# Kernel optimization log

Measured on AMD Instinct MI355X. Metric: run time of the kernel, lower is better.

## Reference

```python
import jax, jax.numpy as jnp
import numpy as np

B, N, D, H = 8, 2048, 128, 8
HD = D // H  # head_depth = 16
CLIP = 10.0
INF = 1e10
THETA = 10000.0
SCALE_BASE = 512.0
LOGIT_SCALE = float(np.log(400.0) / np.log(50.0) / np.sqrt(HD))


def _rotate_half(x):
    # interleaved pairs: (x1, x2) -> (-x2, x1)
    x1 = x[..., ::2]
    x2 = x[..., 1::2]
    return jnp.stack((-x2, x1), axis=-1).reshape(x.shape)


def _rope_xpos(n, hd):
    # rotary_embedding_torch RotaryEmbedding(dim=hd, use_xpos=True)
    inv_freq = 1.0 / (THETA ** (jnp.arange(0, hd, 2, dtype=jnp.float32) / hd))  # (hd/2,)
    t = jnp.arange(n, dtype=jnp.float32)
    freqs = t[:, None] * inv_freq[None, :]          # (n, hd/2)
    freqs = jnp.repeat(freqs, 2, axis=-1)           # (n, hd) interleaved dup
    sc = (jnp.arange(0, hd, 2, dtype=jnp.float32) + 0.4 * hd) / (1.4 * hd)  # (hd/2,)
    power = (t - (n // 2)) / SCALE_BASE             # centered positions
    scale = sc[None, :] ** power[:, None]           # (n, hd/2)
    scale = jnp.repeat(scale, 2, axis=-1)           # (n, hd)
    return freqs, scale


def setup_inputs() -> dict:
    key = jax.random.key(0)
    ks = jax.random.split(key, 7)
    stdv_qkv = 1.0 / np.sqrt(HD)
    stdv_out = 1.0 / np.sqrt(D)
    q = jax.random.normal(ks[0], (B, N, D), dtype=jnp.float32)
    k = jax.random.normal(ks[1], (B, N, D), dtype=jnp.float32)
    v = jax.random.normal(ks[2], (B, N, D), dtype=jnp.float32)
    Wq = jax.random.uniform(ks[3], (D, D), minval=-stdv_qkv, maxval=stdv_qkv, dtype=jnp.float32)
    Wk = jax.random.uniform(ks[4], (D, D), minval=-stdv_qkv, maxval=stdv_qkv, dtype=jnp.float32)
    Wv = jax.random.uniform(ks[5], (D, D), minval=-stdv_qkv, maxval=stdv_qkv, dtype=jnp.float32)
    Wout = jax.random.uniform(ks[6], (D, D), minval=-stdv_out, maxval=stdv_out, dtype=jnp.float32)
    mask = jnp.zeros((B, N, 1), dtype=bool)
    return {"q": q, "k": k, "v": v, "Wq": Wq, "Wk": Wk, "Wv": Wv, "Wout": Wout, "mask": mask}


def reference(q, k, v, Wq, Wk, Wv, Wout, mask):
    def split_heads(t, W):
        # torch Linear (bias=False): t @ W.T, then (B,N,H,HD) -> (B,H,N,HD)
        return (t @ W.T).reshape(B, N, H, HD).transpose(0, 2, 1, 3)

    Qh = split_heads(q, Wq)
    Kh = split_heads(k, Wk)
    Vh = split_heads(v, Wv)

    freqs, scale = _rope_xpos(N, HD)  # (N, HD) each, broadcast over (B,H,N,HD)
    cos, sin = jnp.cos(freqs), jnp.sin(freqs)
    Qr = Qh * (cos * scale) + _rotate_half(Qh) * (sin * scale)
    inv_scale = 1.0 / scale
    Kr = Kh * (cos * inv_scale) + _rotate_half(Kh) * (sin * inv_scale)

    logits = jnp.einsum('bhqd,bhkd->bhqk', Qr, Kr) * LOGIT_SCALE
    logits = CLIP * jnp.tanh(logits)
    # mask: (B,N,1) bool, True -> masked; broadcast to (B,1,1,N)
    logits = jnp.where(mask[:, None, None, :, 0], -INF, logits)
    probs = jax.nn.softmax(logits, axis=-1)
    out = jnp.einsum('bhqk,bhkd->bhqd', probs, Vh)
    out = out.transpose(0, 2, 1, 3).reshape(B, N, D)
    return out @ Wout.T
```

## Files before the change

### kernel.cpp

```cpp
#include <hip/hip_runtime.h>
#include <math.h>

#define BB 8
#define NN 2048
#define DD 128
#define HH 8

typedef _Float16 v4h __attribute__((ext_vector_type(4)));
typedef _Float16 v8h __attribute__((ext_vector_type(8)));
typedef float    v4f __attribute__((ext_vector_type(4)));
typedef float    v16f __attribute__((ext_vector_type(16)));

__device__ __forceinline__ v4f zero4() { v4f z = {0.f, 0.f, 0.f, 0.f}; return z; }
__device__ __forceinline__ v16f zero16() {
    v16f z;
    #pragma unroll
    for (int i = 0; i < 16; ++i) z[i] = 0.f;
    return z;
}

__device__ __forceinline__ v4f mfma16(v4h a, v4h b, v4f c) {
    return __builtin_amdgcn_mfma_f32_16x16x16f16(a, b, c, 0, 0, 0);
}
__device__ __forceinline__ v16f mfma32(v8h a, v8h b, v16f c) {
    return __builtin_amdgcn_mfma_f32_32x32x16_f16(a, b, c, 0, 0, 0);
}

__device__ __forceinline__ float fexp2(float x) {
#if __has_builtin(__builtin_amdgcn_exp2f)
    return __builtin_amdgcn_exp2f(x);
#else
    return __expf(x * 0.69314718055994531f);
#endif
}

#define QSCALE 1.10478088f
#define C1F 14.426950408889634f
#define C2F 28.853900817779268f

__global__ __launch_bounds__(256) void proj_rope_kernel(
    const float* __restrict__ q, const float* __restrict__ k, const float* __restrict__ v,
    const float* __restrict__ Wq, const float* __restrict__ Wk, const float* __restrict__ Wv,
    _Float16* __restrict__ Qr, _Float16* __restrict__ Kr, _Float16* __restrict__ VT)
{
    __shared__ __align__(16) _Float16 xb[64][136];
    __shared__ __align__(16) float ctc[64][16];
    __shared__ __align__(16) float cts[64][16];
    const int tid = threadIdx.x;
    const int m  = blockIdx.y;
    const int r0 = blockIdx.x * 64;
    const int b  = r0 >> 11;
    const int n0 = r0 & 2047;

    const float* s = ((m == 0) ? q : (m == 1) ? k : v) + (size_t)r0 * 128;
    #pragma unroll
    for (int i = 0; i < 8; ++i) {
        int u = tid + i * 256;
        int row = u >> 5, c4 = (u & 31) * 4;
        v4f f = *(const v4f*)(s + row * 128 + c4);
        v4h hv; hv[0]=(_Float16)f[0]; hv[1]=(_Float16)f[1]; hv[2]=(_Float16)f[2]; hv[3]=(_Float16)f[3];
        *(v4h*)&xb[row][c4] = hv;
    }

    if (m < 2) {
        #pragma unroll
        for (int i = 0; i < 2; ++i) {
            int u2 = tid + i * 256;
            int tl = u2 >> 3, j = u2 & 7;
            float fa = (j & 4) ? 1e-2f : 1.f;
            float fb = (j & 2) ? 1e-1f : 1.f;
            float fc = (j & 1) ? 0.31622776601683794f : 1.f;
            float invf = fa * fb * fc;
            float t = (float)(n0 + tl);
            float freq = t * invf;
            float c = cosf(freq), si = sinf(freq);
            float scf = ((float)(2 * j) + 6.4f) / 22.4f;
            float pw  = (t - 1024.0f) / 512.0f;
            float scl = exp2f(pw * log2f(scf));
            float sc  = (m == 0) ? scl * QSCALE : 1.0f / scl;
            float cc = c * sc, ss = si * sc;
            ctc[tl][2 * j]     = cc;
            ctc[tl][2 * j + 1] = cc;
            cts[tl][2 * j]     = ss;
            cts[tl][2 * j + 1] = ss;
        }
    }
    __syncthreads();

    const int w = tid >> 6, lane = tid & 63;
    const int l16 = lane & 15, quad = lane >> 4;

    v4h xf[8];
    #pragma unroll
    for (int kt = 0; kt < 8; ++kt)
        xf[kt] = *(const v4h*)&xb[w * 16 + l16][kt * 16 + quad * 4];
    const float* Wm = (m == 0) ? Wq : (m == 1) ? Wk : Wv;
    v4f acc[8];
    #pragma unroll
    for (int ct = 0; ct < 8; ++ct) acc[ct] = zero4();
    #pragma unroll
    for (int kt = 0; kt < 8; ++kt) {
        #pragma unroll
        for (int ct = 0; ct < 8; ++ct) {
            v4f wv = *(const v4f*)(Wm + (ct * 16 + l16) * 128 + kt * 16 + quad * 4);
            v4h wf; wf[0]=(_Float16)wv[0]; wf[1]=(_Float16)wv[1]; wf[2]=(_Float16)wv[2]; wf[3]=(_Float16)wv[3];
            if (m < 2) acc[ct] = mfma16(wf, xf[kt], acc[ct]);
            else       acc[ct] = mfma16(xf[kt], wf, acc[ct]);
        }
    }
    if (m < 2) {
        const int tl = w * 16 + l16;
        const int n = n0 + tl;
        _Float16* dst = (m == 0 ? Qr : Kr);
        #pragma unroll
        for (int ct = 0; ct < 8; ++ct) {
            v4f cs = *(const v4f*)&ctc[tl][quad * 4];
            v4f sn = *(const v4f*)&cts[tl][quad * 4];
            v4f a = acc[ct];
            v4f rot; rot[0] = -a[1]; rot[1] = a[0]; rot[2] = -a[3]; rot[3] = a[2];
            v4h o;
            #pragma unroll
            for (int r = 0; r < 4; ++r) o[r] = (_Float16)(a[r] * cs[r] + rot[r] * sn[r]);
            *(v4h*)(dst + ((size_t)(b * 8 + ct) * NN + n) * 16 + quad * 4) = o;
        }
    } else {
        const int quadp = (quad == 1) ? 2 : (quad == 2) ? 1 : quad;
        #pragma unroll
        for (int ct = 0; ct < 8; ++ct) {
            v4f a = acc[ct];
            v4h o;
            #pragma unroll
            for (int r = 0; r < 4; ++r) o[r] = (_Float16)a[r];
            *(v4h*)(VT + ((size_t)(b * 8 + ct) * 16 + l16) * NN + n0 + w * 16 + quadp * 4) = o;
        }
    }
}

__global__ __launch_bounds__(256, 4) void attn_kernel(
    const _Float16* __restrict__ Qr, const _Float16* __restrict__ Kr,
    const _Float16* __restrict__ VT, const unsigned char* __restrict__ mask,
    _Float16* __restrict__ Obuf)
{
    __shared__ __align__(16) _Float16 osm[4 * 768];

    const int raw = blockIdx.x;
    const int lb  = (raw & 7) * 128 + (raw >> 3);
    const int bh = lb >> 4;
    const int qt = lb & 15;
    const int b = bh >> 3, h = bh & 7;
    const int q0 = qt * 128;
    const int tid = threadIdx.x;
    const int w = tid >> 6, lane = tid & 63;
    const int l32 = lane & 31, hi = lane >> 5;

    const int qrow = q0 + w * 32 + l32;
    v8h qf = *(const v8h*)(Qr + ((size_t)bh * NN + qrow) * 16 + hi * 8);

    v8h one8;
    #pragma unroll
    for (int i = 0; i < 8; ++i) one8[i] = (_Float16)1.f;

    unsigned long long any4;
    {
        const unsigned long long* mq = (const unsigned long long*)(mask + (size_t)b * NN);
        unsigned long long m0 = mq[lane * 4] | mq[lane * 4 + 1] | mq[lane * 4 + 2] | mq[lane * 4 + 3];
        any4 = __ballot(m0 != 0);
    }

    v16f acc = zero16();
    const _Float16* Kb = Kr + (size_t)bh * NN * 16;
    const _Float16* Vb = VT + ((size_t)bh * 16 + l32) * NN;

    #pragma unroll 1
    for (int it = 0; it < 16; ++it) {
        const int k0 = it * 128;
        const bool mt = ((any4 >> (it * 4)) & 15ull) != 0;

        #pragma unroll
        for (int kc = 0; kc < 4; ++kc) {
            v8h kf = *(const v8h*)(Kb + (size_t)(k0 + kc * 32 + l32) * 16 + hi * 8);
            v8h vfa = one8, vfb = one8;
            if (l32 < 16) {
                vfa = *(const v8h*)(Vb + k0 + kc * 32 + hi * 8);
                vfb = *(const v8h*)(Vb + k0 + kc * 32 + 16 + hi * 8);
            }
            v16f sv = mfma32(kf, qf, zero16());

            float ad[16];
            if (mt) {
                #pragma unroll
                for (int r = 0; r < 16; ++r) {
                    int kk = k0 + kc * 32 + (r >> 2) * 8 + hi * 4 + (r & 3);
                    ad[r] = mask[(size_t)b * NN + kk] ? -1e30f : C1F;
                }
            } else {
                #pragma unroll
                for (int r = 0; r < 16; ++r) ad[r] = C1F;
            }

            float p[16];
            #pragma unroll
            for (int r = 0; r < 16; ++r) {
                float u  = fexp2(sv[r]);
                float rc = __builtin_amdgcn_rcpf(u + 1.f);
                p[r] = fexp2(__builtin_fmaf(rc, -C2F, ad[r]));
            }
            v8h pa0, pa1;
            #pragma unroll
            for (int j = 0; j < 8; ++j) { pa0[j] = (_Float16)p[j]; pa1[j] = (_Float16)p[8 + j]; }
            acc = mfma32(pa0, vfa, acc);
            acc = mfma32(pa1, vfb, acc);
        }
    }

    float rs[16];
    #pragma unroll
    for (int r = 0; r < 16; ++r) rs[r] = __shfl_xor(acc[r], 16, 64);

    _Float16* myOt = osm + w * 768;
    if (!(lane & 16)) {
        int j = lane & 15;
        #pragma unroll
        for (int r = 0; r < 16; ++r) {
            int qr = (r & 3) + 8 * (r >> 2) + 4 * hi;
            myOt[qr * 24 + j] = (_Float16)(acc[r] * __builtin_amdgcn_rcpf(rs[r]));
        }
    }
    asm volatile("s_waitcnt lgkmcnt(0)" ::: "memory");
    v8h ov = *(const v8h*)(myOt + (lane >> 1) * 24 + (lane & 1) * 8);
    *(v8h*)(Obuf + ((size_t)(b * NN + q0 + w * 32 + (lane >> 1)) * 128) + h * 16 + (lane & 1) * 8) = ov;
}

__global__ __launch_bounds__(256) void outproj_kernel(
    const _Float16* __restrict__ Obuf, const float* __restrict__ Wo,
    float* __restrict__ out)
{
    __shared__ __align__(16) _Float16 ob[64][136];
    const int tid = threadIdx.x;
    const int r0 = blockIdx.x * 64;
    const int ct0 = blockIdx.y * 2;
    #pragma unroll
    for (int i = 0; i < 8; ++i) {
        int u = tid + i * 256;
        int row = u >> 5, c4 = (u & 31) * 4;
        *(v4h*)&ob[row][c4] = *(const v4h*)(Obuf + (size_t)(r0 + row) * 128 + c4);
    }
    __syncthreads();
    const int w = tid >> 6, lane = tid & 63;
    const int l16 = lane & 15, quad = lane >> 4;
    v4h af[8];
    #pragma unroll
    for (int kt = 0; kt < 8; ++kt)
        af[kt] = *(const v4h*)&ob[w * 16 + l16][kt * 16 + quad * 4];
    v4f acc[2];
    #pragma unroll
    for (int c = 0; c < 2; ++c) acc[c] = zero4();
    #pragma unroll
    for (int kt = 0; kt < 8; ++kt)
        #pragma unroll
        for (int c = 0; c < 2; ++c) {
            v4f wv = *(const v4f*)(Wo + ((ct0 + c) * 16 + l16) * 128 + kt * 16 + quad * 4);
            v4h wf; wf[0]=(_Float16)wv[0]; wf[1]=(_Float16)wv[1]; wf[2]=(_Float16)wv[2]; wf[3]=(_Float16)wv[3];
            acc[c] = mfma16(af[kt], wf, acc[c]);
        }
    #pragma unroll
    for (int c = 0; c < 2; ++c)
        #pragma unroll
        for (int r = 0; r < 4; ++r)
            out[(size_t)(r0 + w * 16 + quad * 4 + r) * 128 + (ct0 + c) * 16 + l16] = acc[c][r];
}

extern "C" void kernel_launch(void* const* d_in, const int* in_sizes, int n_in,
                              void* d_out, int out_size, void* d_ws, size_t ws_size,
                              hipStream_t stream)
{
    const float* q  = (const float*)d_in[0];
    const float* k  = (const float*)d_in[1];
    const float* v  = (const float*)d_in[2];
    const float* Wq = (const float*)d_in[3];
    const float* Wk = (const float*)d_in[4];
    const float* Wv = (const float*)d_in[5];
    const float* Wo = (const float*)d_in[6];
    const unsigned char* mask = (const unsigned char*)d_in[7];
    float* out = (float*)d_out;

    char* ws = (char*)d_ws;
    _Float16* Qr   = (_Float16*)(ws);
    _Float16* Kr   = (_Float16*)(ws + 4194304);
    _Float16* VTd  = (_Float16*)(ws + 8388608);
    _Float16* Obuf = (_Float16*)(ws + 12582912);

    proj_rope_kernel<<<dim3(256, 3), 256, 0, stream>>>(q, k, v, Wq, Wk, Wv, Qr, Kr, VTd);
    attn_kernel<<<1024, 256, 0, stream>>>(Qr, Kr, VTd, mask, Obuf);
    outproj_kernel<<<dim3(256, 4), 256, 0, stream>>>(Obuf, Wo, out);
}
```

Measured before the change: 204.3 us.

## Stage K and V tiles in shared memory with register prefetch

Result: faster. 195.9 us (-4.1%).

```diff
diff --git a/kernel.cpp b/kernel.cpp
--- a/kernel.cpp
+++ b/kernel.cpp
@@ -141,7 +141,9 @@
     const _Float16* __restrict__ VT, const unsigned char* __restrict__ mask,
     _Float16* __restrict__ Obuf)
 {
-    __shared__ __align__(16) _Float16 osm[4 * 768];
+    __shared__ __align__(16) char smem[14848];
+    _Float16* Kt = (_Float16*)smem;
+    _Float16* Ve = (_Float16*)(smem + 6144);
 
     const int raw = blockIdx.x;
     const int lb  = (raw & 7) * 128 + (raw >> 3);
@@ -156,9 +158,12 @@
     const int qrow = q0 + w * 32 + l32;
     v8h qf = *(const v8h*)(Qr + ((size_t)bh * NN + qrow) * 16 + hi * 8);
 
-    v8h one8;
-    #pragma unroll
-    for (int i = 0; i < 8; ++i) one8[i] = (_Float16)1.f;
+    {
+        v8h one8;
+        #pragma unroll
+        for (int i = 0; i < 8; ++i) one8[i] = (_Float16)1.f;
+        *(v8h*)(Ve + (16 + (tid >> 4)) * 136 + (tid & 15) * 8) = one8;
+    }
 
     unsigned long long any4;
     {
@@ -168,22 +173,33 @@
     }
 
     v16f acc = zero16();
-    const _Float16* Kb = Kr + (size_t)bh * NN * 16;
-    const _Float16* Vb = VT + ((size_t)bh * 16 + l32) * NN;
-
-    #pragma unroll 1
+
+    const int krow = tid >> 1, kpar = tid & 1;
+    const int vhd = tid >> 4, vg = tid & 15;
+    const _Float16* Kbase = Kr + (size_t)bh * NN * 16;
+    const _Float16* Vbase = VT + ((size_t)bh * 16 + vhd) * NN;
+    const unsigned char* mbase = mask + (size_t)b * NN;
+
+    v8h kv = *(const v8h*)(Kbase + (size_t)krow * 16 + kpar * 8);
+    v8h vv = *(const v8h*)(Vbase + vg * 8);
+
     for (int it = 0; it < 16; ++it) {
+        __syncthreads();
+        *(v8h*)(Kt + krow * 24 + kpar * 8) = kv;
+        *(v8h*)(Ve + vhd * 136 + vg * 8) = vv;
+        if (it < 15) {
+            const int k0n = (it + 1) * 128;
+            kv = *(const v8h*)(Kbase + (size_t)(k0n + krow) * 16 + kpar * 8);
+            vv = *(const v8h*)(Vbase + k0n + vg * 8);
+        }
+        __syncthreads();
+
         const int k0 = it * 128;
         const bool mt = ((any4 >> (it * 4)) & 15ull) != 0;
 
         #pragma unroll
         for (int kc = 0; kc < 4; ++kc) {
-            v8h kf = *(const v8h*)(Kb + (size_t)(k0 + kc * 32 + l32) * 16 + hi * 8);
-            v8h vfa = one8, vfb = one8;
-            if (l32 < 16) {
-                vfa = *(const v8h*)(Vb + k0 + kc * 32 + hi * 8);
-                vfb = *(const v8h*)(Vb + k0 + kc * 32 + 16 + hi * 8);
-            }
+            v8h kf = *(const v8h*)(Kt + (kc * 32 + l32) * 24 + hi * 8);
             v16f sv = mfma32(kf, qf, zero16());
 
             float ad[16];
@@ -191,7 +207,7 @@
                 #pragma unroll
                 for (int r = 0; r < 16; ++r) {
                     int kk = k0 + kc * 32 + (r >> 2) * 8 + hi * 4 + (r & 3);
-                    ad[r] = mask[(size_t)b * NN + kk] ? -1e30f : C1F;
+                    ad[r] = mbase[kk] ? -1e30f : C1F;
                 }
             } else {
                 #pragma unroll
@@ -205,11 +221,15 @@
                 float rc = __builtin_amdgcn_rcpf(u + 1.f);
                 p[r] = fexp2(__builtin_fmaf(rc, -C2F, ad[r]));
             }
-            v8h pa0, pa1;
+
             #pragma unroll
-            for (int j = 0; j < 8; ++j) { pa0[j] = (_Float16)p[j]; pa1[j] = (_Float16)p[8 + j]; }
-            acc = mfma32(pa0, vfa, acc);
-            acc = mfma32(pa1, vfb, acc);
+            for (int c2 = 0; c2 < 2; ++c2) {
+                v8h pa;
+                #pragma unroll
+                for (int j = 0; j < 8; ++j) pa[j] = (_Float16)p[c2 * 8 + j];
+                v8h vf = *(const v8h*)(Ve + l32 * 136 + (kc * 2 + c2) * 16 + hi * 8);
+                acc = mfma32(pa, vf, acc);
+            }
         }
     }
 
@@ -217,7 +237,8 @@
     #pragma unroll
     for (int r = 0; r < 16; ++r) rs[r] = __shfl_xor(acc[r], 16, 64);
 
-    _Float16* myOt = osm + w * 768;
+    __syncthreads();
+    _Float16* myOt = (_Float16*)smem + w * 768;
     if (!(lane & 16)) {
         int j = lane & 15;
         #pragma unroll
```
